# Optimization experiments

Measured on AMD Instinct MI355X. Metric: run time of the kernel, lower is better.

Reference implementation:

```python
import jax, jax.numpy as jnp
import numpy as np

T = 48  # top-T from init

def setup_inputs() -> dict:
    key = jax.random.key(0)
    ks = jax.random.split(key, 8)
    B, C, H, W = 16, 512, 32, 32
    tc = C // 8
    return {
        "x": jax.random.normal(ks[0], (B, C, H, W), jnp.float32),
        "fW": jax.random.normal(ks[1], (tc, C), jnp.float32) * 0.05,
        "fb": jax.random.normal(ks[2], (tc,), jnp.float32) * 0.05,
        "gW": jax.random.normal(ks[3], (tc, C), jnp.float32) * 0.05,
        "gb": jax.random.normal(ks[4], (tc,), jnp.float32) * 0.05,
        "hW": jax.random.normal(ks[5], (C, C), jnp.float32) * 0.05,
        "hb": jax.random.normal(ks[6], (C,), jnp.float32) * 0.05,
        "scale": jax.random.normal(ks[7], (1,), jnp.float32),
    }

def reference(x, fW, fb, gW, gb, hW, hb, scale):
    B, C, H, W = x.shape
    tc = fW.shape[0]
    HW = H * W
    # normalize by Frobenius norm over (batch, channel) -> [H, W]
    xn = x / jnp.linalg.norm(x, axis=(0, 1))[None, None]  # [B,C,H,W]
    # 1x1 convs, output already channel-last [B,H,W,out]
    f = jnp.einsum('bchw,oc->bhwo', xn, fW) + fb          # [B,H,W,tc]
    g = jnp.einsum('bchw,oc->bhwo', xn, gW) + gb          # [B,H,W,tc]
    h = jnp.einsum('bchw,oc->bhwo', xn, hW) + hb          # [B,H,W,C]
    xp = jnp.transpose(xn, (0, 2, 3, 1))                  # [B,H,W,C]
    # scores: queries H-major, keys W-major (faithful to permute(0,3,2,1).reshape)
    g_keys = jnp.transpose(g, (0, 3, 2, 1)).reshape(B, tc, HW)  # [B,tc,W*H]
    s = jnp.matmul(f.reshape(B, HW, tc), g_keys)          # [B,HW,HW]
    beta = jax.nn.softmax(s, axis=-1)
    o = jnp.matmul(beta, h.reshape(B, HW, C)).reshape(B, H, W, C)
    fdd = scale * o + xp                                  # [B,H,W,C]
    # per-batch correlation: fdd[b] ([H,W,C]) @ fdd[b].reshape(C,HW)
    corr = jnp.einsum('bhwc,bcn->bhwn', fdd, fdd.reshape(B, C, HW))  # [B,H,W,HW]
    top = jax.lax.top_k(corr, T)[0]                       # descending top-T values
    top = jax.nn.relu(top)
    top = top / jnp.linalg.norm(top, axis=(0, 1))[None, None]  # norm over (B,H) -> [W,T]
    return jnp.transpose(top, (0, 3, 1, 2))               # [B,T,H,W]
```

## Files before the change

kernel.cpp:

```cpp
#include <hip/hip_runtime.h>
#include <cstdint>
#include <cstddef>

#define B_   16
#define C_   512
#define H_   32
#define W_   32
#define HW_  1024
#define TC_  64
#define T_   48

typedef unsigned short u16;
typedef __attribute__((ext_vector_type(8))) short short8v;
typedef __attribute__((ext_vector_type(4))) float f32x4;

__device__ __forceinline__ u16 tobf(float x) {
    unsigned u = __float_as_uint(x);
    return (u16)((u + 0x7FFFu + ((u >> 16) & 1u)) >> 16);
}
__device__ __forceinline__ float frombf(u16 h) {
    return __uint_as_float(((unsigned)h) << 16);
}

__device__ __forceinline__ void gld16(const void* g, void* l) {
    __builtin_amdgcn_global_load_lds(
        (const __attribute__((address_space(1))) void*)g,
        (__attribute__((address_space(3))) void*)l, 16, 0, 0);
}

__global__ void k_colsq(const float* __restrict__ x, float* __restrict__ partial) {
    int bid = blockIdx.x;
    int col = (bid & 3) * 256 + threadIdx.x;
    int r0  = (bid >> 2) * 128;
    const float* p = x + (size_t)r0 * HW_ + col;
    float s = 0.f;
    for (int r = 0; r < 128; ++r) { float v = p[(size_t)r * HW_]; s += v * v; }
    partial[(size_t)(bid >> 2) * HW_ + col] = s;
}

__global__ void k_rsqrt(const float* __restrict__ partial, float* __restrict__ ninv) {
    int i = blockIdx.x * 256 + threadIdx.x;
    if (i < HW_) {
        float s = 0.f;
        for (int r = 0; r < 64; ++r) s += partial[(size_t)r * HW_ + i];
        ninv[i] = rsqrtf(s);
    }
}

__global__ void k_transpose(const float* __restrict__ x, const float* __restrict__ ninv,
                            u16* __restrict__ obH) {
    __shared__ float tile[32][33];
    int b  = blockIdx.z;
    int m0 = blockIdx.x * 32, c0 = blockIdx.y * 32;
    int tx = threadIdx.x, ty = threadIdx.y;
    const float* xb = x + (size_t)b * C_ * HW_;
    #pragma unroll
    for (int j = 0; j < 32; j += 8)
        tile[ty + j][tx] = xb[(size_t)(c0 + ty + j) * HW_ + m0 + tx];
    __syncthreads();
    size_t base = (size_t)b * HW_ * C_;
    #pragma unroll
    for (int j = 0; j < 32; j += 8) {
        int m = m0 + ty + j;
        obH[base + (size_t)m * C_ + c0 + tx] = tobf(tile[tx][ty + j] * ninv[m]);
    }
}

__global__ void k_packW(const float* __restrict__ in, u16* __restrict__ oh) {
    size_t i = (size_t)blockIdx.x * 256 + threadIdx.x;
    oh[i] = tobf(in[i]);
}
__global__ void k_packFG(const float* __restrict__ fW, const float* __restrict__ gW,
                         const float* __restrict__ fb, const float* __restrict__ gb,
                         u16* __restrict__ oh, float* __restrict__ fgb) {
    int idx = blockIdx.x * 256 + threadIdx.x;
    int row = idx >> 9, c = idx & 511;
    float v = (row < 64) ? fW[row * 512 + c] : gW[(row - 64) * 512 + c];
    oh[idx] = tobf(v);
    if (idx < 128) fgb[idx] = (idx < 64) ? fb[idx] : gb[idx - 64];
}

template<int EPI>
__global__ __launch_bounds__(256) void k_gemm1(
    const u16* __restrict__ A, const u16* __restrict__ Bm,
    const float* __restrict__ bias,
    float* __restrict__ Cf, u16* __restrict__ Ch,
    const float* __restrict__ scaleP,
    int N, int K, int lda, int ldb, long sA, long sB, long sC)
{
    __shared__ u16 lds[3 * 8192];
    const int gx = gridDim.x, gy = gridDim.y, gz = gridDim.z;
    int bidl = blockIdx.x + gx * (blockIdx.y + gy * blockIdx.z);
    int nwg = gx * gy * gz;
    int sw = (bidl & 7) * (nwg >> 3) + (bidl >> 3);
    int gxy = gx * gy;
    int bz = sw / gxy, rem = sw - bz * gxy;
    int by = rem / gx, bx = rem - by * gx;

    const int b = bz;
    const u16* pA = A + (size_t)b * sA;
    const u16* pB = Bm + (size_t)b * sB;
    const int m0 = by * 128, n0 = bx * 128;
    const int tid = threadIdx.x, wave = tid >> 6, lane = tid & 63;
    const int wm = wave >> 1, wn = wave & 1;
    const int g = lane >> 4;

    f32x4 acc[4][4];
    #pragma unroll
    for (int i = 0; i < 4; ++i)
        #pragma unroll
        for (int j = 0; j < 4; ++j) { f32x4 z = {0.f,0.f,0.f,0.f}; acc[i][j] = z; }

    auto STAGE = [&](int kt, int buf) {
        const int k0 = kt << 5;
        u16* lb = lds + buf * 8192;
        #pragma unroll
        for (int q = 0; q < 4; ++q) {
            int ci = wave * 4 + q;
            bool isA = ci < 8;
            int li = ci & 7;
            const u16* gp = isA ? pA : pB;
            int ld = isA ? lda : ldb;
            int rb = isA ? m0 : n0;
            int rp = li * 8 + (lane >> 3);
            int gg = (lane & 7) ^ (rp & 7);
            int r  = rp * 2 + (gg >> 2);
            int kc = k0 + (gg & 3) * 8;
            gld16(gp + (size_t)(rb + r) * ld + kc,
                  lb + (isA ? 0 : 4096) + li * 512 + lane * 8);
        }
    };
    auto COMPUTE = [&](int buf) {
        const u16* As = lds + buf * 8192;
        const u16* Bs = As + 4096;
        short8v av[4];
        #pragma unroll
        for (int i = 0; i < 4; ++i) {
            int r = wm * 64 + i * 16 + (lane & 15);
            int rp = r >> 1, gg = ((r & 1) << 2) + g;
            av[i] = *(const short8v*)(As + rp * 64 + ((gg ^ (rp & 7)) << 3));
        }
        #pragma unroll
        for (int j = 0; j < 4; ++j) {
            int r = wn * 64 + j * 16 + (lane & 15);
            int rp = r >> 1, gg = ((r & 1) << 2) + g;
            short8v bv = *(const short8v*)(Bs + rp * 64 + ((gg ^ (rp & 7)) << 3));
            #pragma unroll
            for (int i = 0; i < 4; ++i)
                acc[i][j] = __builtin_amdgcn_mfma_f32_16x16x32_bf16(av[i], bv, acc[i][j], 0, 0, 0);
        }
    };

    const int nkt = K >> 5;
    STAGE(0, 0);
    STAGE(1, 1);
    int cur = 0;
    for (int kt = 0; kt < nkt; ++kt) {
        int nxt2 = cur + 2; if (nxt2 >= 3) nxt2 -= 3;
        if (kt + 2 < nkt) {
            STAGE(kt + 2, nxt2);
            asm volatile("s_waitcnt vmcnt(8)" ::: "memory");
        } else if (kt + 1 < nkt) {
            asm volatile("s_waitcnt vmcnt(4)" ::: "memory");
        } else {
            asm volatile("s_waitcnt vmcnt(0)" ::: "memory");
        }
        __builtin_amdgcn_s_barrier();
        __builtin_amdgcn_sched_barrier(0);
        COMPUTE(cur);
        __builtin_amdgcn_sched_barrier(0);
        __builtin_amdgcn_s_barrier();
        ++cur; if (cur >= 3) cur -= 3;
    }

    const float sc = (EPI == 2) ? scaleP[0] : 0.f;
    const int colbase = n0 + wn * 64 + (lane & 15);
    const int rowbase = m0 + wm * 64 + ((lane >> 4) << 2);
    #pragma unroll
    for (int i = 0; i < 4; ++i)
        #pragma unroll
        for (int j = 0; j < 4; ++j) {
            int col = colbase + j * 16;
            #pragma unroll
            for (int rg = 0; rg < 4; ++rg) {
                int row = rowbase + i * 16 + rg;
                size_t idx = (size_t)b * sC + (size_t)row * N + col;
                float a = acc[i][j][rg];
                if (EPI == 0)      Cf[idx] = a;
                else if (EPI == 2) Ch[idx] = tobf(sc * a + frombf(Ch[idx]));
                else if (EPI == 5) Ch[idx] = tobf(a + bias[row]);
                else               Ch[idx] = tobf(a + bias[col]);
            }
        }
}

__global__ __launch_bounds__(512) void k_ssoft(
    const u16* __restrict__ fg,
    u16* __restrict__ P)
{
    __shared__ u16 lds[69632];
    __shared__ float red[512];
    __shared__ float rowm[64];
    __shared__ float rinv[64];

    const int b = blockIdx.y;
    const int m0 = blockIdx.x * 64;
    const u16* fgb = fg + (size_t)b * 131072;
    const int tid = threadIdx.x, wave = tid >> 6, lane = tid & 63;
    const int wn = wave;
    const int g = lane >> 4;

    #pragma unroll
    for (int kc = 0; kc < 2; ++kc) {
        #pragma unroll
        for (int q = 0; q < 8; ++q) {
            int li = wave * 8 + q;
            int rp = li * 8 + (lane >> 3);
            int gg = (lane & 7) ^ (rp & 7);
            int r  = rp * 2 + (gg >> 2);
            int n2 = ((r & 31) << 5) | (r >> 5);
            int kcol = 64 + kc * 32 + (gg & 3) * 8;
            gld16(fgb + (size_t)n2 * 128 + kcol,
                  lds + 4096 + kc * 32768 + li * 512 + lane * 8);
        }
        if (lane < 32) {
            int rp = wave * 4 + (lane >> 3);
            int gg = (lane & 7) ^ (rp & 7);
            int r  = rp * 2 + (gg >> 2);
            int kcol = kc * 32 + (gg & 3) * 8;
            gld16(fgb + (size_t)(m0 + r) * 128 + kcol,
                  lds + kc * 2048 + wave * 256 + lane * 8);
        }
    }
    __syncthreads();

    f32x4 acc[4][8];
    #pragma unroll
    for (int i = 0; i < 4; ++i)
        #pragma unroll
        for (int j = 0; j < 8; ++j) { f32x4 z = {0.f,0.f,0.f,0.f}; acc[i][j] = z; }

    #pragma unroll
    for (int kc = 0; kc < 2; ++kc) {
        const u16* As = lds + kc * 2048;
        const u16* Bs = lds + 4096 + kc * 32768;
        short8v av[4];
        #pragma unroll
        for (int i = 0; i < 4; ++i) {
            int r = i * 16 + (lane & 15);
            int rp = r >> 1, gg = ((r & 1) << 2) + g;
            av[i] = *(const short8v*)(As + rp * 64 + ((gg ^ (rp & 7)) << 3));
        }
        #pragma unroll
        for (int j = 0; j < 8; ++j) {
            int n = wn * 128 + j * 16 + (lane & 15);
            int rp = n >> 1, gg = ((n & 1) << 2) + g;
            short8v bv = *(const short8v*)(Bs + rp * 64 + ((gg ^ (rp & 7)) << 3));
            #pragma unroll
            for (int i = 0; i < 4; ++i)
                acc[i][j] = __builtin_amdgcn_mfma_f32_16x16x32_bf16(av[i], bv, acc[i][j], 0, 0, 0);
        }
    }

    const int rgrp = (lane >> 4) << 2;
    float pm[4][4];
    #pragma unroll
    for (int i = 0; i < 4; ++i)
        #pragma unroll
        for (int rg = 0; rg < 4; ++rg) {
            float m = acc[i][0][rg];
            #pragma unroll
            for (int j = 1; j < 8; ++j) m = fmaxf(m, acc[i][j][rg]);
            pm[i][rg] = m;
        }
    #pragma unroll
    for (int o = 1; o < 16; o <<= 1)
        #pragma unroll
        for (int i = 0; i < 4; ++i)
            #pragma unroll
            for (int rg = 0; rg < 4; ++rg)
                pm[i][rg] = fmaxf(pm[i][rg], __shfl_xor(pm[i][rg], o));
    if ((lane & 15) == 0)
        #pragma unroll
        for (int i = 0; i < 4; ++i)
            #pragma unroll
            for (int rg = 0; rg < 4; ++rg)
                red[wn * 64 + i * 16 + rgrp + rg] = pm[i][rg];
    __syncthreads();
    if (tid < 64) {
        float m = red[tid];
        #pragma unroll
        for (int w = 1; w < 8; ++w) m = fmaxf(m, red[w * 64 + tid]);
        rowm[tid] = m;
    }
    __syncthreads();

    float ps[4][4];
    #pragma unroll
    for (int i = 0; i < 4; ++i)
        #pragma unroll
        for (int rg = 0; rg < 4; ++rg) {
            float m = rowm[i * 16 + rgrp + rg];
            float s = 0.f;
            #pragma unroll
            for (int j = 0; j < 8; ++j) {
                float e = expf(acc[i][j][rg] - m);
                acc[i][j][rg] = e;
                s += e;
            }
            ps[i][rg] = s;
        }
    #pragma unroll
    for (int o = 1; o < 16; o <<= 1)
        #pragma unroll
        for (int i = 0; i < 4; ++i)
            #pragma unroll
            for (int rg = 0; rg < 4; ++rg)
                ps[i][rg] += __shfl_xor(ps[i][rg], o);
    if ((lane & 15) == 0)
        #pragma unroll
        for (int i = 0; i < 4; ++i)
            #pragma unroll
            for (int rg = 0; rg < 4; ++rg)
                red[wn * 64 + i * 16 + rgrp + rg] = ps[i][rg];
    __syncthreads();
    if (tid < 64) {
        float s = red[tid];
        #pragma unroll
        for (int w = 1; w < 8; ++w) s += red[w * 64 + tid];
        rinv[tid] = 1.f / s;
    }
    __syncthreads();

    u16* Plds = lds + 4096;
    #pragma unroll
    for (int i = 0; i < 4; ++i)
        #pragma unroll
        for (int rg = 0; rg < 4; ++rg) {
            int r = i * 16 + rgrp + rg;
            float riv = rinv[r];
            int sx = (r & 7) << 4;
            #pragma unroll
            for (int j = 0; j < 8; ++j) {
                u16 v = tobf(acc[i][j][rg] * riv);
                int col = wn * 128 + ((j * 16) ^ sx) + (lane & 15);
                Plds[r * 1024 + col] = v;
            }
        }
    __syncthreads();

    for (int it = 0; it < 16; ++it) {
        int r  = it * 4 + (tid >> 7);
        int cb = (tid & 127) * 8;
        int sx = (r & 7) << 4;
        int src = r * 1024 + (cb & ~127) + ((cb & 127) ^ sx);
        short8v v = *(const short8v*)(Plds + src);
        *(short8v*)(P + ((size_t)b * HW_ + m0 + r) * (size_t)HW_ + cb) = v;
    }
}

__global__ void k_tposeU1(const u16* __restrict__ src, u16* __restrict__ dst) {
    __shared__ u16 tile[32][33];
    int b = blockIdx.z;
    const u16* sb = src + (size_t)b * (C_ * HW_);
    u16* db = dst + (size_t)b * (C_ * HW_);
    int c0 = blockIdx.x * 32, r0 = blockIdx.y * 32;
    int tx = threadIdx.x, ty = threadIdx.y;
    #pragma unroll
    for (int j = 0; j < 32; j += 8)
        tile[ty + j][tx] = sb[(size_t)(r0 + ty + j) * HW_ + c0 + tx];
    __syncthreads();
    #pragma unroll
    for (int j = 0; j < 32; j += 8)
        db[(size_t)(c0 + ty + j) * C_ + r0 + tx] = tile[tx][ty + j];
}

__device__ __forceinline__ float sort64_desc(float v, int lane) {
    #pragma unroll
    for (int k = 2; k <= 64; k <<= 1) {
        #pragma unroll
        for (int j = k >> 1; j > 0; j >>= 1) {
            float o = __shfl_xor(v, j);
            bool takeMax = (((lane & k) == 0) == ((lane & j) == 0));
            v = takeMax ? fmaxf(v, o) : fminf(v, o);
        }
    }
    return v;
}
__device__ __forceinline__ float bmerge64_desc(float a, float b, int lane) {
    float br = __shfl(b, 63 - lane);
    float c = fmaxf(a, br);
    #pragma unroll
    for (int j = 32; j > 0; j >>= 1) {
        float o = __shfl_xor(c, j);
        c = ((lane & j) == 0) ? fmaxf(c, o) : fminf(c, o);
    }
    return c;
}

__global__ __launch_bounds__(256) void k_topk(const float* __restrict__ corr,
                                              float* __restrict__ topv) {
    __shared__ float buf[4][1024];
    int wave = threadIdx.x >> 6, lane = threadIdx.x & 63;
    int row = blockIdx.x * 4 + wave;
    const float4* rp = (const float4*)(corr + (size_t)row * HW_);

    float4 e[4];
    #pragma unroll
    for (int q = 0; q < 4; ++q) e[q] = rp[lane * 4 + q];

    float gm = -INFINITY;
    #pragma unroll
    for (int q = 0; q < 4; ++q)
        gm = fmaxf(gm, fmaxf(fmaxf(e[q].x, e[q].y), fmaxf(e[q].z, e[q].w)));
    float sorted = sort64_desc(gm, lane);
    float tau = __shfl(sorted, T_ - 1);

    int c = 0;
    #pragma unroll
    for (int q = 0; q < 4; ++q)
        c += (e[q].x >= tau) + (e[q].y >= tau) + (e[q].z >= tau) + (e[q].w >= tau);
    int sc = c;
    #pragma unroll
    for (int o = 1; o < 64; o <<= 1) {
        int t2 = __shfl_up(sc, o);
        if (lane >= o) sc += t2;
    }
    int off = sc - c;
    int cnt = __shfl(sc, 63);

    float* wb = buf[wave];
    #pragma unroll
    for (int q = 0; q < 4; ++q) {
        if (e[q].x >= tau) wb[off++] = e[q].x;
        if (e[q].y >= tau) wb[off++] = e[q].y;
        if (e[q].z >= tau) wb[off++] = e[q].z;
        if (e[q].w >= tau) wb[off++] = e[q].w;
    }

    float* orow = topv + (size_t)row * T_;
    if (cnt <= 64) {
        float a = (lane < cnt) ? wb[lane] : -INFINITY;
        a = sort64_desc(a, lane);
        if (lane < T_) orow[lane] = fmaxf(a, 0.f);
    } else if (cnt <= 128) {
        float a  = sort64_desc(wb[lane], lane);
        float b2 = sort64_desc((lane < cnt - 64) ? wb[64 + lane] : -INFINITY, lane);
        float m2 = bmerge64_desc(a, b2, lane);
        if (lane < T_) orow[lane] = fmaxf(m2, 0.f);
    } else {
        int P = 256; while (P < cnt) P <<= 1;
        for (int i = cnt + lane; i < P; i += 64) wb[i] = -INFINITY;
        for (int k = 2; k <= P; k <<= 1)
            for (int j = k >> 1; j > 0; j >>= 1)
                for (int t2 = lane; t2 < P; t2 += 64) {
                    int ixj = t2 ^ j;
                    if (ixj > t2) {
                        float a = wb[t2], b3 = wb[ixj];
                        bool desc = ((t2 & k) == 0);
                        if (desc ? (a < b3) : (a > b3)) { wb[t2] = b3; wb[ixj] = a; }
                    }
                }
        if (lane < T_) orow[lane] = fmaxf(wb[lane], 0.f);
    }
}

__global__ void k_colss(const float* __restrict__ topv, float* __restrict__ colss) {
    int o = blockIdx.x;
    int w = o / T_, t = o % T_;
    int lane = threadIdx.x;
    float s = 0.f;
    for (int i = lane; i < 512; i += 64) {
        int b = i >> 5, h = i & 31;
        float v = topv[(size_t)((b << 10) + (h << 5) + w) * T_ + t];
        s += v * v;
    }
    for (int off = 32; off > 0; off >>= 1) s += __shfl_down(s, off);
    if (lane == 0) colss[o] = s;
}

__global__ void k_final(const float* __restrict__ topv, const float* __restrict__ colss,
                        float* __restrict__ out) {
    int idx = blockIdx.x * 256 + threadIdx.x;
    if (idx >= B_ * T_ * HW_) return;
    int w = idx & 31;
    int h = (idx >> 5) & 31;
    int t = (idx >> 10) % T_;
    int b = idx / (T_ * HW_);
    float v = topv[(size_t)((b << 10) + (h << 5) + w) * T_ + t];
    out[idx] = v * rsqrtf(colss[w * T_ + t]);
}

extern "C" void kernel_launch(void* const* d_in, const int* in_sizes, int n_in,
                              void* d_out, int out_size, void* d_ws, size_t ws_size,
                              hipStream_t stream) {
    const float* x     = (const float*)d_in[0];
    const float* fW    = (const float*)d_in[1];
    const float* fb    = (const float*)d_in[2];
    const float* gW    = (const float*)d_in[3];
    const float* gb    = (const float*)d_in[4];
    const float* hW    = (const float*)d_in[5];
    const float* hb    = (const float*)d_in[6];
    const float* scale = (const float*)d_in[7];
    float* out = (float*)d_out;

    char* wsb = (char*)d_ws;
    float* part = (float*)(wsb + 0);
    float* ninv = (float*)(wsb + 262144);
    u16*   hWh  = (u16*)(wsb + 266240);
    u16*   fgWh = (u16*)(wsb + 790528);
    float* fgb  = (float*)(wsb + 921600);
    u16*   xnH  = (u16*)(wsb + 922112);
    u16*   fgH  = (u16*)(wsb + 17699328);
    u16*   fgL  = (u16*)(wsb + 21893632);
    u16*   hvTH = (u16*)(wsb + 26087936);
    float* S    = (float*)(wsb + 42865152);
    float* topv = (float*)fgH;
    float* colss= (float*)fgL;
    u16*   Sp   = (u16*)S;

    const long sXn = 524288;
    const long sFG = 131072;
    const long sS  = 1048576;

    k_colsq<<<256, 256, 0, stream>>>(x, part);
    k_rsqrt<<<4, 256, 0, stream>>>(part, ninv);

    k_transpose<<<dim3(32, 16, 16), dim3(32, 8), 0, stream>>>(x, ninv, xnH);

    k_packW<<<1024, 256, 0, stream>>>(hW, hWh);
    k_packFG<<<256, 256, 0, stream>>>(fW, gW, fb, gb, fgWh, fgb);

    k_gemm1<6><<<dim3(1, 8, 16), 256, 0, stream>>>(
        xnH, fgWh, fgb, nullptr, fgH, nullptr,
        128, 512, 512, 512, sXn, 0, sFG);

    k_gemm1<5><<<dim3(8, 4, 16), 256, 0, stream>>>(
        hWh, xnH, hb, nullptr, hvTH, nullptr,
        1024, 512, 512, 512, 0, sXn, sXn);

    k_ssoft<<<dim3(16, 16), 512, 0, stream>>>(fgH, Sp);

    k_gemm1<2><<<dim3(4, 8, 16), 256, 0, stream>>>(
        Sp, hvTH, nullptr, nullptr, xnH, scale,
        512, 1024, 1024, 1024, sS, sXn, sXn);

    k_tposeU1<<<dim3(32, 16, 16), dim3(32, 8), 0, stream>>>(xnH, hvTH);

    k_gemm1<0><<<dim3(8, 8, 16), 256, 0, stream>>>(
        xnH, hvTH, nullptr, S, nullptr, nullptr,
        1024, 512, 512, 512, sXn, sXn, sS);

    k_topk<<<B_ * HW_ / 4, 256, 0, stream>>>(S, topv);

    k_colss<<<W_ * T_, 64, 0, stream>>>(topv, colss);
    k_final<<<(B_ * T_ * HW_ + 255) / 256, 256, 0, stream>>>(topv, colss, out);
}
```

Baseline: 195.4 us.

## Fuse fdd transpose into attention-output GEMM epilogue and use double-buffered LDS

The attention-output GEMM epilogue now also writes its result tile in transposed layout through LDS into a new buffer, so the separate transpose kernel and its global round trip are removed. The GEMM mainloop drops from a 3-stage to a 2-stage LDS pipeline (prefetch distance 1) to free the LDS needed for the transposed staging. This may expose more memory latency in every GEMM instantiation in exchange for eliminating one kernel launch and a full read/write pass.

```diff
diff --git a/kernel.cpp b/kernel.cpp
--- a/kernel.cpp
+++ b/kernel.cpp
@@ -84,11 +84,11 @@
 __global__ __launch_bounds__(256) void k_gemm1(
     const u16* __restrict__ A, const u16* __restrict__ Bm,
     const float* __restrict__ bias,
-    float* __restrict__ Cf, u16* __restrict__ Ch,
+    float* __restrict__ Cf, u16* __restrict__ Ch, u16* __restrict__ Ct,
     const float* __restrict__ scaleP,
     int N, int K, int lda, int ldb, long sA, long sB, long sC)
 {
-    __shared__ u16 lds[3 * 8192];
+    __shared__ u16 lds[18432];
     const int gx = gridDim.x, gy = gridDim.y, gz = gridDim.z;
     int bidl = blockIdx.x + gx * (blockIdx.y + gy * blockIdx.z);
     int nwg = gx * gy * gz;
@@ -153,14 +153,10 @@
 
     const int nkt = K >> 5;
     STAGE(0, 0);
-    STAGE(1, 1);
     int cur = 0;
     for (int kt = 0; kt < nkt; ++kt) {
-        int nxt2 = cur + 2; if (nxt2 >= 3) nxt2 -= 3;
-        if (kt + 2 < nkt) {
-            STAGE(kt + 2, nxt2);
-            asm volatile("s_waitcnt vmcnt(8)" ::: "memory");
-        } else if (kt + 1 < nkt) {
+        if (kt + 1 < nkt) {
+            STAGE(kt + 1, cur ^ 1);
             asm volatile("s_waitcnt vmcnt(4)" ::: "memory");
         } else {
             asm volatile("s_waitcnt vmcnt(0)" ::: "memory");
@@ -170,10 +166,10 @@
         COMPUTE(cur);
         __builtin_amdgcn_sched_barrier(0);
         __builtin_amdgcn_s_barrier();
-        ++cur; if (cur >= 3) cur -= 3;
-    }
-
-    const float sc = (EPI == 2) ? scaleP[0] : 0.f;
+        cur ^= 1;
+    }
+
+    const float sc = (EPI == 7) ? scaleP[0] : 0.f;
     const int colbase = n0 + wn * 64 + (lane & 15);
     const int rowbase = m0 + wm * 64 + ((lane >> 4) << 2);
     #pragma unroll
@@ -187,11 +183,28 @@
                 size_t idx = (size_t)b * sC + (size_t)row * N + col;
                 float a = acc[i][j][rg];
                 if (EPI == 0)      Cf[idx] = a;
-                else if (EPI == 2) Ch[idx] = tobf(sc * a + frombf(Ch[idx]));
                 else if (EPI == 5) Ch[idx] = tobf(a + bias[row]);
-                else               Ch[idx] = tobf(a + bias[col]);
+                else if (EPI == 6) Ch[idx] = tobf(a + bias[col]);
+                else {
+                    u16 v = tobf(sc * a + frombf(Ch[idx]));
+                    Ch[idx] = v;
+                    int lr = row - m0, lc = col - n0;
+                    lds[(size_t)((lr & 1) * 128 + lc) * 72 + (lr >> 1)] = v;
+                }
             }
         }
+
+    if (EPI == 7) {
+        __syncthreads();
+        #pragma unroll
+        for (int it = 0; it < 8; ++it) {
+            int task = it * 256 + tid;
+            int tc = task >> 3, ch = task & 7;
+            short8v v = *(const short8v*)(lds + tc * 72 + ch * 8);
+            int cg = ((tc >> 7) ? 512 : 0) + n0 + (tc & 127);
+            *(short8v*)(Ct + (size_t)b * 524288 + (size_t)cg * 512 + (m0 >> 1) + ch * 8) = v;
+        }
+    }
 }
 
 __global__ __launch_bounds__(512) void k_ssoft(
@@ -357,22 +370,6 @@
         short8v v = *(const short8v*)(Plds + src);
         *(short8v*)(P + ((size_t)b * HW_ + m0 + r) * (size_t)HW_ + cb) = v;
     }
-}
-
-__global__ void k_tposeU1(const u16* __restrict__ src, u16* __restrict__ dst) {
-    __shared__ u16 tile[32][33];
-    int b = blockIdx.z;
-    const u16* sb = src + (size_t)b * (C_ * HW_);
-    u16* db = dst + (size_t)b * (C_ * HW_);
-    int c0 = blockIdx.x * 32, r0 = blockIdx.y * 32;
-    int tx = threadIdx.x, ty = threadIdx.y;
-    #pragma unroll
-    for (int j = 0; j < 32; j += 8)
-        tile[ty + j][tx] = sb[(size_t)(r0 + ty + j) * HW_ + c0 + tx];
-    __syncthreads();
-    #pragma unroll
-    for (int j = 0; j < 32; j += 8)
-        db[(size_t)(c0 + ty + j) * C_ + r0 + tx] = tile[tx][ty + j];
 }
 
 __device__ __forceinline__ float sort64_desc(float v, int lane) {
@@ -515,6 +512,7 @@
     u16*   fgL  = (u16*)(wsb + 21893632);
     u16*   hvTH = (u16*)(wsb + 26087936);
     float* S    = (float*)(wsb + 42865152);
+    u16*   fddT = (u16*)(wsb + 109974016);
     float* topv = (float*)fgH;
     float* colss= (float*)fgL;
     u16*   Sp   = (u16*)S;
@@ -532,23 +530,21 @@
     k_packFG<<<256, 256, 0, stream>>>(fW, gW, fb, gb, fgWh, fgb);
 
     k_gemm1<6><<<dim3(1, 8, 16), 256, 0, stream>>>(
-        xnH, fgWh, fgb, nullptr, fgH, nullptr,
+        xnH, fgWh, fgb, nullptr, fgH, nullptr, nullptr,
         128, 512, 512, 512, sXn, 0, sFG);
 
     k_gemm1<5><<<dim3(8, 4, 16), 256, 0, stream>>>(
-        hWh, xnH, hb, nullptr, hvTH, nullptr,
+        hWh, xnH, hb, nullptr, hvTH, nullptr, nullptr,
         1024, 512, 512, 512, 0, sXn, sXn);
 
     k_ssoft<<<dim3(16, 16), 512, 0, stream>>>(fgH, Sp);
 
-    k_gemm1<2><<<dim3(4, 8, 16), 256, 0, stream>>>(
-        Sp, hvTH, nullptr, nullptr, xnH, scale,
+    k_gemm1<7><<<dim3(4, 8, 16), 256, 0, stream>>>(
+        Sp, hvTH, nullptr, nullptr, xnH, fddT, scale,
         512, 1024, 1024, 1024, sS, sXn, sXn);
 
-    k_tposeU1<<<dim3(32, 16, 16), dim3(32, 8), 0, stream>>>(xnH, hvTH);
-
     k_gemm1<0><<<dim3(8, 8, 16), 256, 0, stream>>>(
-        xnH, hvTH, nullptr, S, nullptr, nullptr,
+        xnH, fddT, nullptr, S, nullptr, nullptr, nullptr,
         1024, 512, 512, 512, sXn, sXn, sS);
 
     k_topk<<<B_ * HW_ / 4, 256, 0, stream>>>(S, topv);
```

After: 186.3 us. -4.6%, faster.
